# Kernel tuning notes

Hardware: AMD Instinct MI355X
Metric: run time of the kernel (lower is better)

The kernel has to match this reference:

```python
import jax, jax.numpy as jnp
import numpy as np

B, S, D, H = 2, 2048, 1024, 16
HD = D // H


def setup_inputs() -> dict:
    key = jax.random.key(0)
    ks = jax.random.split(key, 12)
    sc = 0.02
    inp = {
        "q": jax.random.normal(ks[0], (B, S, D), jnp.float32),
        "k": jax.random.normal(ks[1], (B, S, D), jnp.float32),
        "v": jax.random.normal(ks[2], (B, S, D), jnp.float32),
        # causal mask, broadcastable to [B,H,S,S]; 0 => masked
        "mask": jnp.tril(jnp.ones((S, S), jnp.int32))[None, None],
        "Wq": jax.random.normal(ks[3], (D, D), jnp.float32) * sc,
        "bq": jnp.zeros((D,), jnp.float32),
        "Wk": jax.random.normal(ks[4], (D, D), jnp.float32) * sc,
        "bk": jnp.zeros((D,), jnp.float32),
        "Wv": jax.random.normal(ks[5], (D, D), jnp.float32) * sc,
        "bv": jnp.zeros((D,), jnp.float32),
        "Wf": jax.random.normal(ks[6], (D, D), jnp.float32) * sc,
        "bf": jnp.zeros((D,), jnp.float32),
    }
    return inp


def reference(q, k, v, mask, Wq, bq, Wk, bk, Wv, bv, Wf, bf):
    b = q.shape[0]
    # projections (torch Linear: x @ W.T + b)
    qh = (q @ Wq.T + bq).reshape(b, -1, H, HD).transpose(0, 2, 1, 3)  # [B,H,S,HD]
    kh = (k @ Wk.T + bk).reshape(b, -1, H, HD).transpose(0, 2, 1, 3)
    vh = (v @ Wv.T + bv).reshape(b, -1, H, HD).transpose(0, 2, 1, 3)
    scores = jnp.einsum("bhqd,bhkd->bhqk", qh, kh) / jnp.sqrt(jnp.float32(HD))
    scores = jnp.where(mask == 0, jnp.float32(-1e9), scores)
    attn = jax.nn.softmax(scores, axis=-1)
    x = jnp.einsum("bhqk,bhkd->bhqd", attn, vh)  # [B,H,S,HD]
    x = x.transpose(0, 2, 1, 3).reshape(b, -1, D)
    return x @ Wf.T + bf
```

## Files before the change

kernel.cpp:

```cpp
#include <hip/hip_runtime.h>
#include <hip/hip_bf16.h>

typedef __attribute__((ext_vector_type(4))) float f32x4;
typedef __attribute__((ext_vector_type(8))) short bf16x8;
typedef unsigned short u16;
typedef unsigned int u32;

#define QSCALE 0.18033688011112042f
#define MASKVAL (-60.0f)

__device__ __forceinline__ u16 f2bf(float f) {
  union { float f; u32 u; } v; v.f = f;
  u32 r = v.u + 0x7fffu + ((v.u >> 16) & 1u);
  return (u16)(r >> 16);
}

__device__ __forceinline__ u32 cvtpk(float a, float b) {
  u32 r;
  asm("v_cvt_pk_bf16_f32 %0, %1, %2" : "=v"(r) : "v"(a), "v"(b));
  return r;
}

__device__ __forceinline__ u32 cvtpk_safe(float a, float b) {
  __hip_bfloat162 h = __float22bfloat162_rn(float2{a, b});
  union { __hip_bfloat162 h; u32 u; } v; v.h = h;
  return v.u;
}

__device__ __forceinline__ float nexp2(float x) {
  return __builtin_amdgcn_exp2f(x);
}

__device__ __forceinline__ void gl_lds16(const u16* g, u16* l) {
  __builtin_amdgcn_global_load_lds((const __attribute__((address_space(1))) u32*)g,
                                   (__attribute__((address_space(3))) u32*)l, 16, 0, 0);
}

__global__ __launch_bounds__(256) void conv_kernel(
    const float* __restrict__ q, const float* __restrict__ k, const float* __restrict__ v,
    const float* __restrict__ wq, const float* __restrict__ wk, const float* __restrict__ wv,
    const float* __restrict__ wf, u16* __restrict__ dst)
{
  size_t i = ((size_t)blockIdx.x * 256 + threadIdx.x) * 8;
  const float* src; size_t off;
  if (i < ((size_t)3 << 22)) {
    int a = (int)(i >> 22);
    src = (a == 0) ? q : ((a == 1) ? k : v);
    off = i & ((1u << 22) - 1);
  } else {
    size_t j = i - ((size_t)3 << 22);
    int a = (int)(j >> 20);
    src = (a == 0) ? wq : ((a == 1) ? wk : ((a == 2) ? wv : wf));
    off = j & ((1u << 20) - 1);
  }
  float4 x0 = *reinterpret_cast<const float4*>(src + off);
  float4 x1 = *reinterpret_cast<const float4*>(src + off + 4);
  u32 o[4] = {cvtpk(x0.x, x0.y), cvtpk(x0.z, x0.w), cvtpk(x1.x, x1.y), cvtpk(x1.z, x1.w)};
  *reinterpret_cast<uint4*>(dst + i) = *reinterpret_cast<const uint4*>(o);
}

struct GArg {
  const u16* X; const u16* W; const float* bias; void* out; int mode; float scale;
};

template<int BM>
__global__ __launch_bounds__(256) void gemm_bf(GArg a0, GArg a1, GArg a2) {
  constexpr int K = 1024, N = 1024;
  constexpr int WNw = (BM == 128) ? 2 : 4;
  constexpr int NI  = (128 / WNw) / 16;
  constexpr int CA  = BM / 32;
  __shared__ __align__(16) u16 lA[BM * 64];
  __shared__ __align__(16) u16 lB[128 * 64];
  GArg a = (blockIdx.z == 0) ? a0 : ((blockIdx.z == 1) ? a1 : a2);
  const int m0 = blockIdx.x * BM, n0 = blockIdx.y * 128;
  const int tid = threadIdx.x, w = tid >> 6, lane = tid & 63;
  const int lr = lane & 15, lg = lane >> 4;
  const int wm = (w / WNw) * 64, wn = (w % WNw) * (128 / WNw);
  const int lrow8 = lane >> 3, lc = lane & 7;
  const int schunk = (lc ^ lrow8) * 8;

  f32x4 acc[4][NI] = {};

  for (int kt = 0; kt < K; kt += 64) {
    #pragma unroll
    for (int c = 0; c < CA; ++c) {
      int row = w * (BM / 4) + c * 8 + lrow8;
      gl_lds16(a.X + (size_t)(m0 + row) * K + kt + schunk, &lA[(w * (BM / 4) + c * 8) * 64]);
    }
    #pragma unroll
    for (int c = 0; c < 4; ++c) {
      int row = w * 32 + c * 8 + lrow8;
      gl_lds16(a.W + (size_t)(n0 + row) * K + kt + schunk, &lB[(w * 32 + c * 8) * 64]);
    }
    __syncthreads();
    #pragma unroll
    for (int h = 0; h < 2; ++h) {
      bf16x8 af[4], bfv[NI];
      #pragma unroll
      for (int i = 0; i < 4; ++i) {
        int r = wm + i * 16 + lr;
        af[i] = *reinterpret_cast<const bf16x8*>(&lA[r * 64 + (((h * 4 + lg) ^ (r & 7)) * 8)]);
      }
      #pragma unroll
      for (int i = 0; i < NI; ++i) {
        int r = wn + i * 16 + lr;
        bfv[i] = *reinterpret_cast<const bf16x8*>(&lB[r * 64 + (((h * 4 + lg) ^ (r & 7)) * 8)]);
      }
      __builtin_amdgcn_s_setprio(1);
      #pragma unroll
      for (int mi = 0; mi < 4; ++mi)
        #pragma unroll
        for (int ni = 0; ni < NI; ++ni)
          acc[mi][ni] = __builtin_amdgcn_mfma_f32_16x16x32_bf16(af[mi], bfv[ni], acc[mi][ni], 0, 0, 0);
      __builtin_amdgcn_s_setprio(0);
    }
    __syncthreads();
  }

  #pragma unroll
  for (int mi = 0; mi < 4; ++mi) {
    #pragma unroll
    for (int ni = 0; ni < NI; ++ni) {
      int col = n0 + wn + ni * 16 + lr;
      float bv = a.bias[col];
      #pragma unroll
      for (int r = 0; r < 4; ++r) {
        int row = m0 + wm + mi * 16 + lg * 4 + r;
        float val = (acc[mi][ni][r] + bv) * a.scale;
        if (a.mode == 2) {
          ((float*)a.out)[(size_t)row * N + col] = val;
        } else {
          int b = row >> 11, s = row & 2047, hh = col >> 6, hd = col & 63;
          u16* O = (u16*)a.out;
          if (a.mode == 0) O[((size_t)(b * 16 + hh) * 2048 + s) * 64 + hd] = f2bf(val);
          else             O[((size_t)(b * 16 + hh) * 64 + hd) * 2048 + s] = f2bf(val);
        }
      }
    }
  }
}

template<int IN_BF16, int OUT_MODE>
__global__ __launch_bounds__(256) void gemm_legacy(
    const void* __restrict__ Xv, const float* __restrict__ W,
    const float* __restrict__ bias, void* __restrict__ Outv, float scale)
{
  constexpr int N = 1024, K = 1024;
  __shared__ __align__(16) u16 lA[128 * 32];
  __shared__ __align__(16) u16 lB[128 * 32];
  const int n0 = blockIdx.x * 128, m0 = blockIdx.y * 128;
  const int tid = threadIdx.x;
  const int w = tid >> 6, lane = tid & 63, lr = lane & 15, lg = lane >> 4;
  const int wm = (w >> 1) * 64, wn = (w & 1) * 64;
  f32x4 acc[4][4] = {};
  for (int kt = 0; kt < K; kt += 32) {
    #pragma unroll
    for (int it = 0; it < 4; ++it) {
      int idx = it * 256 + tid, row = idx >> 3, c4 = idx & 7;
      float4 xv = *reinterpret_cast<const float4*>(&W[(size_t)(n0 + row) * K + kt + c4 * 4]);
      u16* dst = &lB[row * 32 + c4 * 4];
      dst[0] = f2bf(xv.x); dst[1] = f2bf(xv.y); dst[2] = f2bf(xv.z); dst[3] = f2bf(xv.w);
    }
    if (IN_BF16 == 0) {
      const float* X = (const float*)Xv;
      #pragma unroll
      for (int it = 0; it < 4; ++it) {
        int idx = it * 256 + tid, row = idx >> 3, c4 = idx & 7;
        float4 xv = *reinterpret_cast<const float4*>(&X[(size_t)(m0 + row) * K + kt + c4 * 4]);
        u16* dst = &lA[row * 32 + c4 * 4];
        dst[0] = f2bf(xv.x); dst[1] = f2bf(xv.y); dst[2] = f2bf(xv.z); dst[3] = f2bf(xv.w);
      }
    } else {
      const u16* X = (const u16*)Xv;
      #pragma unroll
      for (int it = 0; it < 2; ++it) {
        int idx = it * 256 + tid, row = idx >> 2, c = idx & 3;
        *reinterpret_cast<uint4*>(&lA[row * 32 + c * 8]) =
            *reinterpret_cast<const uint4*>(&X[(size_t)(m0 + row) * K + kt + c * 8]);
      }
    }
    __syncthreads();
    bf16x8 af[4], bfr[4];
    #pragma unroll
    for (int i = 0; i < 4; ++i) {
      af[i]  = *reinterpret_cast<const bf16x8*>(&lA[(wm + i * 16 + lr) * 32 + lg * 8]);
      bfr[i] = *reinterpret_cast<const bf16x8*>(&lB[(wn + i * 16 + lr) * 32 + lg * 8]);
    }
    #pragma unroll
    for (int mi = 0; mi < 4; ++mi)
      #pragma unroll
      for (int ni = 0; ni < 4; ++ni)
        acc[mi][ni] = __builtin_amdgcn_mfma_f32_16x16x32_bf16(af[mi], bfr[ni], acc[mi][ni], 0, 0, 0);
    __syncthreads();
  }
  #pragma unroll
  for (int mi = 0; mi < 4; ++mi)
    #pragma unroll
    for (int ni = 0; ni < 4; ++ni) {
      int col = n0 + wn + ni * 16 + lr;
      float bv = bias[col];
      #pragma unroll
      for (int r = 0; r < 4; ++r) {
        int row = m0 + wm + mi * 16 + lg * 4 + r;
        float val = (acc[mi][ni][r] + bv) * scale;
        if (OUT_MODE == 2) {
          ((float*)Outv)[(size_t)row * N + col] = val;
        } else {
          int b = row >> 11, s = row & 2047, h = col >> 6, hd = col & 63;
          u16* O = (u16*)Outv;
          if (OUT_MODE == 0) O[((size_t)(b * 16 + h) * 2048 + s) * 64 + hd] = f2bf(val);
          else               O[((size_t)(b * 16 + h) * 64 + hd) * 2048 + s] = f2bf(val);
        }
      }
    }
}


__device__ __forceinline__ void seg_step4(
    const bf16x8* aq, f32x4* oacc, float& ls,
    const u16* lK, const u16* lV, char* pwb,
    bool diag, int col0, int qv, int lr, int lg, bf16x8 ones)
{
  const int cs = lr & 7;
  f32x4 sc[4];
  #pragma unroll
  for (int nf = 0; nf < 4; ++nf) {
    const u16* kr = &lK[(nf * 16 + lr) * 64];
    bf16x8 k0 = *reinterpret_cast<const bf16x8*>(&kr[(lg ^ cs) * 8]);
    bf16x8 k1 = *reinterpret_cast<const bf16x8*>(&kr[((4 + lg) ^ cs) * 8]);
    f32x4 z = {};
    __builtin_amdgcn_s_setprio(1);
    z = __builtin_amdgcn_mfma_f32_16x16x32_bf16(k0, aq[0], z, 0, 0, 0);
    z = __builtin_amdgcn_mfma_f32_16x16x32_bf16(k1, aq[1], z, 0, 0, 0);
    __builtin_amdgcn_s_setprio(0);
    sc[nf] = z;
  }
  if (diag) {
    #pragma unroll
    for (int nf = 0; nf < 4; ++nf)
      #pragma unroll
      for (int r = 0; r < 4; ++r)
        if ((col0 + nf * 16 + lg * 4 + r) > qv) sc[nf][r] = MASKVAL;
  }
  #pragma unroll
  for (int nf = 0; nf < 4; ++nf) {
    float p0 = nexp2(sc[nf][0]), p1 = nexp2(sc[nf][1]);
    float p2 = nexp2(sc[nf][2]), p3 = nexp2(sc[nf][3]);
    uint2 pr;
    pr.x = cvtpk_safe(p0, p1);
    pr.y = cvtpk_safe(p2, p3);
    *reinterpret_cast<uint2*>(pwb + lr * 128 + ((32 * nf + 8 * lg) ^ (cs << 4))) = pr;
  }
  bf16x8 pb0 = *reinterpret_cast<const bf16x8*>(pwb + lr * 128 + 16 * (lg ^ cs));
  bf16x8 pb1 = *reinterpret_cast<const bf16x8*>(pwb + lr * 128 + 16 * ((4 + lg) ^ cs));
  f32x4 rs = {};
  rs = __builtin_amdgcn_mfma_f32_16x16x32_bf16(ones, pb0, rs, 0, 0, 0);
  rs = __builtin_amdgcn_mfma_f32_16x16x32_bf16(ones, pb1, rs, 0, 0, 0);
  ls += rs[0];
  #pragma unroll
  for (int df = 0; df < 4; ++df) {
    const u16* vr = &lV[(df * 16 + lr) * 64];
    bf16x8 v0 = *reinterpret_cast<const bf16x8*>(&vr[(lg ^ cs) * 8]);
    bf16x8 v1 = *reinterpret_cast<const bf16x8*>(&vr[((4 + lg) ^ cs) * 8]);
    __builtin_amdgcn_s_setprio(1);
    oacc[df] = __builtin_amdgcn_mfma_f32_16x16x32_bf16(v0, pb0, oacc[df], 0, 0, 0);
    oacc[df] = __builtin_amdgcn_mfma_f32_16x16x32_bf16(v1, pb1, oacc[df], 0, 0, 0);
    __builtin_amdgcn_s_setprio(0);
  }
}

__global__ __launch_bounds__(256) void attn_kernel8(
    const u16* __restrict__ Qh, const u16* __restrict__ Kh,
    const u16* __restrict__ Vt, u16* __restrict__ Oa)
{
  __shared__ __align__(16) u16 lK[2][64 * 64];
  __shared__ __align__(16) u16 lV[2][64 * 64];
  __shared__ __align__(16) u16 lP[4][16 * 64];
  const int bh = blockIdx.x;
  const int t = 31 - blockIdx.y;
  const int b = bh >> 4, h = bh & 15;
  const u16* Qb = Qh + (size_t)bh * 2048 * 64;
  const u16* Kb = Kh + (size_t)bh * 2048 * 64;
  const u16* Vb = Vt + (size_t)bh * 64 * 2048;
  const int tid = threadIdx.x, w = tid >> 6, lane = tid & 63;
  const int lr = lane & 15, lg = lane >> 4;
  const int lrow8 = lane >> 3, lc = lane & 7;
  const int schunk = (lc ^ lrow8) * 8;
  char* pwb = (char*)lP[w];

  bf16x8 ones;
  #pragma unroll
  for (int j = 0; j < 8; ++j) ones[j] = (short)0x3F80;

  bf16x8 aq[2];
  {
    int qrow = t * 64 + w * 16 + lr;
    aq[0] = *reinterpret_cast<const bf16x8*>(&Qb[(size_t)qrow * 64 + lg * 8]);
    aq[1] = *reinterpret_cast<const bf16x8*>(&Qb[(size_t)qrow * 64 + 32 + lg * 8]);
  }
  f32x4 oacc[4] = {};
  float ls = 0.f;
  const int qv = t * 64 + w * 16 + lr;

  const int nkt = t + 1;
  int cur = 0;

  #pragma unroll
  for (int c = 0; c < 2; ++c) {
    int row = w * 16 + c * 8 + lrow8;
    gl_lds16(Kb + (size_t)row * 64 + schunk, &lK[0][(w * 16 + c * 8) * 64]);
    gl_lds16(Vb + (size_t)row * 2048 + schunk, &lV[0][(w * 16 + c * 8) * 64]);
  }
  __syncthreads();

  for (int kt = 0; kt < nkt; ++kt) {
    if (kt + 1 < nkt) {
      #pragma unroll
      for (int c = 0; c < 2; ++c) {
        int row = w * 16 + c * 8 + lrow8;
        gl_lds16(Kb + (size_t)((kt + 1) * 64 + row) * 64 + schunk, &lK[cur ^ 1][(w * 16 + c * 8) * 64]);
        gl_lds16(Vb + (size_t)row * 2048 + (kt + 1) * 64 + schunk, &lV[cur ^ 1][(w * 16 + c * 8) * 64]);
      }
    }
    seg_step4(aq, oacc, ls, lK[cur], lV[cur], pwb, kt == t, kt * 64, qv, lr, lg, ones);
    if (kt + 1 < nkt) __syncthreads();
    cur ^= 1;
  }

  float inv = 1.0f / ls;
  #pragma unroll
  for (int df = 0; df < 4; ++df) {
    uint2 pa;
    pa.x = cvtpk(oacc[df][0] * inv, oacc[df][1] * inv);
    pa.y = cvtpk(oacc[df][2] * inv, oacc[df][3] * inv);
    *reinterpret_cast<uint2*>(&Oa[(size_t)(b * 2048 + qv) * 1024 + h * 64 + df * 16 + lg * 4]) = pa;
  }
}

extern "C" void kernel_launch(void* const* d_in, const int* in_sizes, int n_in,
                              void* d_out, int out_size, void* d_ws, size_t ws_size,
                              hipStream_t stream) {
  const float* q  = (const float*)d_in[0];
  const float* k  = (const float*)d_in[1];
  const float* v  = (const float*)d_in[2];
  const float* Wq = (const float*)d_in[4];
  const float* bq = (const float*)d_in[5];
  const float* Wk = (const float*)d_in[6];
  const float* bk = (const float*)d_in[7];
  const float* Wv = (const float*)d_in[8];
  const float* bv = (const float*)d_in[9];
  const float* Wf = (const float*)d_in[10];
  const float* bf = (const float*)d_in[11];

  if (ws_size >= ((size_t)64 << 20)) {
    u16* wsb = (u16*)d_ws;
    u16* qb  = wsb;
    u16* kb  = wsb + (1u << 22);
    u16* vb  = wsb + ((size_t)2 << 22);
    u16* wqb = wsb + ((size_t)3 << 22);
    u16* wkb = wqb + (1u << 20);
    u16* wvb = wkb + (1u << 20);
    u16* wfb = wvb + (1u << 20);
    u16* Qh  = wsb + ((size_t)1 << 24);
    u16* Kh  = Qh + (1u << 22);
    u16* Vt  = Kh + (1u << 22);
    u16* Oa  = Vt + (1u << 22);

    conv_kernel<<<8192, 256, 0, stream>>>(q, k, v, Wq, Wk, Wv, Wf, wsb);

    GArg gq{qb, wqb, bq, Qh, 0, QSCALE};
    GArg gk{kb, wkb, bk, Kh, 0, 1.0f};
    GArg gv{vb, wvb, bv, Vt, 1, 1.0f};
    gemm_bf<128><<<dim3(32, 8, 3), 256, 0, stream>>>(gq, gk, gv);

    attn_kernel8<<<dim3(32, 32), 256, 0, stream>>>(Qh, Kh, Vt, Oa);

    GArg gf{Oa, wfb, bf, d_out, 2, 1.0f};
    gemm_bf<64><<<dim3(64, 8, 1), 256, 0, stream>>>(gf, gf, gf);
  } else {
    u16* Qh = (u16*)d_ws;
    u16* Kh = Qh + (size_t)4096 * 1024;
    u16* Vt = Kh + (size_t)4096 * 1024;
    u16* Oa = Vt + (size_t)4096 * 1024;
    dim3 gg(8, 32), gb(256);
    gemm_legacy<0, 0><<<gg, gb, 0, stream>>>(q, Wq, bq, Qh, QSCALE);
    gemm_legacy<0, 0><<<gg, gb, 0, stream>>>(k, Wk, bk, Kh, 1.0f);
    gemm_legacy<0, 1><<<gg, gb, 0, stream>>>(v, Wv, bv, Vt, 1.0f);
    attn_kernel8<<<dim3(32, 32), gb, 0, stream>>>(Qh, Kh, Vt, Oa);
    gemm_legacy<1, 2><<<gg, gb, 0, stream>>>(Oa, Wf, bf, (float*)d_out, 1.0f);
  }
}
```

Before: 108.8 us.

## Halve attention KV tile to 32 keys and interleave causal tile order

The attention kernel now streams 32-key K/V tiles instead of 64, with smaller LDS buffers, a single P·V MFMA per head-dim fragment and V fragments hoisted ahead of the softmax. The query-tile order across blockIdx.y is also changed from strictly descending to an interleaved long/short pattern, to balance causal work across CUs. This doubles loop iterations and barriers and drops the XOR swizzle on V and P LDS accesses, which may add bank conflicts in exchange for less LDS use and possibly higher occupancy. The diagonal masking now covers the last two 32-wide tiles.

```diff
diff --git a/kernel.cpp b/kernel.cpp
--- a/kernel.cpp
+++ b/kernel.cpp
@@ -216,15 +216,15 @@
 }
 
 
-__device__ __forceinline__ void seg_step4(
+__device__ __forceinline__ void seg_step5(
     const bf16x8* aq, f32x4* oacc, float& ls,
     const u16* lK, const u16* lV, char* pwb,
     bool diag, int col0, int qv, int lr, int lg, bf16x8 ones)
 {
   const int cs = lr & 7;
-  f32x4 sc[4];
-  #pragma unroll
-  for (int nf = 0; nf < 4; ++nf) {
+  f32x4 sc[2];
+  #pragma unroll
+  for (int nf = 0; nf < 2; ++nf) {
     const u16* kr = &lK[(nf * 16 + lr) * 64];
     bf16x8 k0 = *reinterpret_cast<const bf16x8*>(&kr[(lg ^ cs) * 8]);
     bf16x8 k1 = *reinterpret_cast<const bf16x8*>(&kr[((4 + lg) ^ cs) * 8]);
@@ -235,49 +235,46 @@
     __builtin_amdgcn_s_setprio(0);
     sc[nf] = z;
   }
+  bf16x8 va[4];
+  #pragma unroll
+  for (int df = 0; df < 4; ++df)
+    va[df] = *reinterpret_cast<const bf16x8*>(&lV[(df * 16 + lr) * 32 + lg * 8]);
   if (diag) {
     #pragma unroll
-    for (int nf = 0; nf < 4; ++nf)
+    for (int nf = 0; nf < 2; ++nf)
       #pragma unroll
       for (int r = 0; r < 4; ++r)
         if ((col0 + nf * 16 + lg * 4 + r) > qv) sc[nf][r] = MASKVAL;
   }
   #pragma unroll
-  for (int nf = 0; nf < 4; ++nf) {
-    float p0 = nexp2(sc[nf][0]), p1 = nexp2(sc[nf][1]);
-    float p2 = nexp2(sc[nf][2]), p3 = nexp2(sc[nf][3]);
+  for (int nf = 0; nf < 2; ++nf) {
     uint2 pr;
-    pr.x = cvtpk_safe(p0, p1);
-    pr.y = cvtpk_safe(p2, p3);
-    *reinterpret_cast<uint2*>(pwb + lr * 128 + ((32 * nf + 8 * lg) ^ (cs << 4))) = pr;
-  }
-  bf16x8 pb0 = *reinterpret_cast<const bf16x8*>(pwb + lr * 128 + 16 * (lg ^ cs));
-  bf16x8 pb1 = *reinterpret_cast<const bf16x8*>(pwb + lr * 128 + 16 * ((4 + lg) ^ cs));
+    pr.x = cvtpk_safe(nexp2(sc[nf][0]), nexp2(sc[nf][1]));
+    pr.y = cvtpk_safe(nexp2(sc[nf][2]), nexp2(sc[nf][3]));
+    *reinterpret_cast<uint2*>(pwb + lr * 64 + nf * 32 + lg * 8) = pr;
+  }
+  bf16x8 pb = *reinterpret_cast<const bf16x8*>(pwb + lr * 64 + lg * 16);
   f32x4 rs = {};
-  rs = __builtin_amdgcn_mfma_f32_16x16x32_bf16(ones, pb0, rs, 0, 0, 0);
-  rs = __builtin_amdgcn_mfma_f32_16x16x32_bf16(ones, pb1, rs, 0, 0, 0);
+  rs = __builtin_amdgcn_mfma_f32_16x16x32_bf16(ones, pb, rs, 0, 0, 0);
   ls += rs[0];
   #pragma unroll
   for (int df = 0; df < 4; ++df) {
-    const u16* vr = &lV[(df * 16 + lr) * 64];
-    bf16x8 v0 = *reinterpret_cast<const bf16x8*>(&vr[(lg ^ cs) * 8]);
-    bf16x8 v1 = *reinterpret_cast<const bf16x8*>(&vr[((4 + lg) ^ cs) * 8]);
     __builtin_amdgcn_s_setprio(1);
-    oacc[df] = __builtin_amdgcn_mfma_f32_16x16x32_bf16(v0, pb0, oacc[df], 0, 0, 0);
-    oacc[df] = __builtin_amdgcn_mfma_f32_16x16x32_bf16(v1, pb1, oacc[df], 0, 0, 0);
+    oacc[df] = __builtin_amdgcn_mfma_f32_16x16x32_bf16(va[df], pb, oacc[df], 0, 0, 0);
     __builtin_amdgcn_s_setprio(0);
   }
 }
 
-__global__ __launch_bounds__(256) void attn_kernel8(
+__global__ __launch_bounds__(256) void attn_kernel13(
     const u16* __restrict__ Qh, const u16* __restrict__ Kh,
     const u16* __restrict__ Vt, u16* __restrict__ Oa)
 {
-  __shared__ __align__(16) u16 lK[2][64 * 64];
-  __shared__ __align__(16) u16 lV[2][64 * 64];
-  __shared__ __align__(16) u16 lP[4][16 * 64];
+  __shared__ __align__(16) u16 lK[2][32 * 64];
+  __shared__ __align__(16) u16 lV[2][64 * 32];
+  __shared__ __align__(16) u16 lP[4][16 * 32];
   const int bh = blockIdx.x;
-  const int t = 31 - blockIdx.y;
+  const int y = blockIdx.y;
+  const int t = (y < 8) ? (31 - y) : ((y < 16) ? (y - 8) : ((y < 24) ? (39 - y) : (y - 16)));
   const int b = bh >> 4, h = bh & 15;
   const u16* Qb = Qh + (size_t)bh * 2048 * 64;
   const u16* Kb = Kh + (size_t)bh * 2048 * 64;
@@ -302,27 +299,21 @@
   float ls = 0.f;
   const int qv = t * 64 + w * 16 + lr;
 
-  const int nkt = t + 1;
+  const int nkt = 2 * t + 2;
+  const int vrow = w * 16 + (lane >> 2);
+  const int vchunk = (lane & 3) * 8;
   int cur = 0;
 
-  #pragma unroll
-  for (int c = 0; c < 2; ++c) {
-    int row = w * 16 + c * 8 + lrow8;
-    gl_lds16(Kb + (size_t)row * 64 + schunk, &lK[0][(w * 16 + c * 8) * 64]);
-    gl_lds16(Vb + (size_t)row * 2048 + schunk, &lV[0][(w * 16 + c * 8) * 64]);
-  }
+  gl_lds16(Kb + (size_t)(w * 8 + lrow8) * 64 + schunk, &lK[0][(w * 8) * 64]);
+  gl_lds16(Vb + (size_t)vrow * 2048 + vchunk, &lV[0][(w * 16) * 32]);
   __syncthreads();
 
   for (int kt = 0; kt < nkt; ++kt) {
     if (kt + 1 < nkt) {
-      #pragma unroll
-      for (int c = 0; c < 2; ++c) {
-        int row = w * 16 + c * 8 + lrow8;
-        gl_lds16(Kb + (size_t)((kt + 1) * 64 + row) * 64 + schunk, &lK[cur ^ 1][(w * 16 + c * 8) * 64]);
-        gl_lds16(Vb + (size_t)row * 2048 + (kt + 1) * 64 + schunk, &lV[cur ^ 1][(w * 16 + c * 8) * 64]);
-      }
-    }
-    seg_step4(aq, oacc, ls, lK[cur], lV[cur], pwb, kt == t, kt * 64, qv, lr, lg, ones);
+      gl_lds16(Kb + (size_t)((kt + 1) * 32 + w * 8 + lrow8) * 64 + schunk, &lK[cur ^ 1][(w * 8) * 64]);
+      gl_lds16(Vb + (size_t)vrow * 2048 + (kt + 1) * 32 + vchunk, &lV[cur ^ 1][(w * 16) * 32]);
+    }
+    seg_step5(aq, oacc, ls, lK[cur], lV[cur], pwb, kt >= 2 * t, kt * 32, qv, lr, lg, ones);
     if (kt + 1 < nkt) __syncthreads();
     cur ^= 1;
   }
@@ -373,7 +364,7 @@
     GArg gv{vb, wvb, bv, Vt, 1, 1.0f};
     gemm_bf<128><<<dim3(32, 8, 3), 256, 0, stream>>>(gq, gk, gv);
 
-    attn_kernel8<<<dim3(32, 32), 256, 0, stream>>>(Qh, Kh, Vt, Oa);
+    attn_kernel13<<<dim3(32, 32), 256, 0, stream>>>(Qh, Kh, Vt, Oa);
 
     GArg gf{Oa, wfb, bf, d_out, 2, 1.0f};
     gemm_bf<64><<<dim3(64, 8, 1), 256, 0, stream>>>(gf, gf, gf);
@@ -386,7 +377,7 @@
     gemm_legacy<0, 0><<<gg, gb, 0, stream>>>(q, Wq, bq, Qh, QSCALE);
     gemm_legacy<0, 0><<<gg, gb, 0, stream>>>(k, Wk, bk, Kh, 1.0f);
     gemm_legacy<0, 1><<<gg, gb, 0, stream>>>(v, Wv, bv, Vt, 1.0f);
-    attn_kernel8<<<dim3(32, 32), gb, 0, stream>>>(Qh, Kh, Vt, Oa);
+    attn_kernel13<<<dim3(32, 32), gb, 0, stream>>>(Qh, Kh, Vt, Oa);
     gemm_legacy<1, 2><<<gg, gb, 0, stream>>>(Oa, Wf, bf, (float*)d_out, 1.0f);
   }
 }
```

Result: slower. 127.2 us (+16.9%).
